# Optimization experiments

Hardware: AMD Instinct MI355X
Metric: run time of the kernel (lower is better)

Reference implementation:

```python
import jax, jax.numpy as jnp
import numpy as np

NUM_EXPERTS = 8
TOP_K = 2
HIDDEN = 768
FFN = 3072
B, S = 4, 4096


def setup_inputs() -> dict:
    key = jax.random.key(0)
    ks = jax.random.split(key, 7)
    scale_h = 1.0 / np.sqrt(HIDDEN)
    scale_f = 1.0 / np.sqrt(FFN)
    return {
        "hidden_states": jax.random.normal(ks[0], (B, S, HIDDEN), dtype=jnp.float32),
        "router_w": jax.random.normal(ks[1], (HIDDEN, NUM_EXPERTS), dtype=jnp.float32) * scale_h,
        "router_b": jnp.zeros((NUM_EXPERTS,), dtype=jnp.float32),
        "w1": jax.random.normal(ks[2], (NUM_EXPERTS, HIDDEN, FFN), dtype=jnp.float32) * scale_h,
        "b1": jnp.zeros((NUM_EXPERTS, FFN), dtype=jnp.float32),
        "w2": jax.random.normal(ks[3], (NUM_EXPERTS, FFN, HIDDEN), dtype=jnp.float32) * scale_f,
        "b2": jnp.zeros((NUM_EXPERTS, HIDDEN), dtype=jnp.float32),
    }


def _moe_forward(x_flat, router_w, router_b, w1, b1, w2, b2):
    T = x_flat.shape[0]
    # Router: logits [T, E]
    router_logits = x_flat @ router_w + router_b
    routing_weights = jax.nn.softmax(router_logits, axis=-1)
    # Top-k gating: softmax over the selected top-k logits
    top_vals, top_idx = jax.lax.top_k(router_logits, TOP_K)
    top_gates = jax.nn.softmax(top_vals, axis=-1)
    # Scatter gates into dense dispatch mask [T, E]
    rows = jnp.arange(T)[:, None]
    dispatch_mask = jnp.zeros_like(routing_weights).at[rows, top_idx].set(top_gates)
    # Expert computation: combined = sum_e gate[:, e] * FFN_e(x)
    # (tokens with zero gate contribute exactly 0, matching the torch scatter-combine)
    combined = jnp.zeros_like(x_flat)
    for e in range(NUM_EXPERTS):
        h = jax.nn.gelu(x_flat @ w1[e] + b1[e])  # [T, FFN]
        y = h @ w2[e] + b2[e]                    # [T, HIDDEN]
        combined = combined + dispatch_mask[:, e:e + 1] * y
    # Auxiliary load-balancing loss
    mean_routing_prob = jnp.mean(routing_weights, axis=0)
    tokens_per_expert = jnp.sum(dispatch_mask, axis=0) / T
    aux_loss = jnp.sum(mean_routing_prob * tokens_per_expert) * NUM_EXPERTS
    return combined, routing_weights, dispatch_mask, aux_loss, router_logits


def reference(hidden_states, router_w, router_b, w1, b1, w2, b2):
    batch, seq, hid = hidden_states.shape
    x_flat = hidden_states.reshape(-1, hid)
    combined, routing_weights, dispatch_mask, aux_loss, router_logits = _moe_forward(
        x_flat, router_w, router_b, w1, b1, w2, b2)
    E = NUM_EXPERTS
    return (
        combined.reshape(batch, seq, hid),            # expert_outputs
        routing_weights.reshape(batch, seq, E),       # routing_weights
        dispatch_mask.reshape(batch, seq, E),         # dispatch_mask
        aux_loss,                                     # aux_loss
        router_logits.reshape(batch, seq, E),         # router_logits
    )
```

## Files before the change

kernel.cpp:

```cpp
#include <hip/hip_runtime.h>
#include <math.h>

#define TOKENS 16384
#define HID 768
#define FFN_DIM 3072
#define NEXP 8
#define MAXT 136

#define RT_TPB 128
#define RT_BLOCKS (TOKENS / RT_TPB)

typedef __bf16 bf16x8 __attribute__((ext_vector_type(8)));
typedef float f32x4 __attribute__((ext_vector_type(4)));

#define GLOBAL_AS(p) ((const __attribute__((address_space(1))) void*)(p))
#define LDS_AS(p)    ((__attribute__((address_space(3))) void*)(p))

__device__ __forceinline__ float gelu_f(float x) {
    const float x3 = x * x * x;
    const float z = 0.7978845608028654f * (x + 0.044715f * x3);
    const float e = __expf(2.f * z);
    const float t = 1.f - 2.f / (e + 1.f);
    return 0.5f * x * (1.f + t);
}

__device__ __forceinline__ unsigned short f2bf(float v) {
    return __builtin_bit_cast(unsigned short, (__bf16)v);
}

__global__ void __launch_bounds__(512) router_kernel(
    const float* __restrict__ x, const float* __restrict__ rw,
    const float* __restrict__ rb,
    float* __restrict__ out_rw, float* __restrict__ out_dm,
    float* __restrict__ out_logits,
    int* __restrict__ counts, float* __restrict__ probsum,
    float* __restrict__ gatesum, int* __restrict__ lists,
    float* __restrict__ glists)
{
    __shared__ int s_cnt[NEXP], s_base[NEXP];
    __shared__ float s_prob[NEXP], s_gate[NEXP];
    __shared__ int s_e1[RT_TPB], s_s1[RT_TPB], s_e2[RT_TPB], s_s2[RT_TPB];
    __shared__ float s_g1v[RT_TPB], s_g2v[RT_TPB];

    const int tid = threadIdx.x;
    if (tid < NEXP) { s_cnt[tid] = 0; s_prob[tid] = 0.f; s_gate[tid] = 0.f; }
    __syncthreads();

    const int wave = tid >> 6, lane = tid & 63;

    for (int it = 0; it < RT_TPB / 8; ++it) {
        const int lt = wave * (RT_TPB / 8) + it;
        const int t = blockIdx.x * RT_TPB + lt;
        const float* xr = x + (size_t)t * HID;
        float acc[NEXP];
#pragma unroll
        for (int e = 0; e < NEXP; ++e) acc[e] = 0.f;
#pragma unroll
        for (int j = 0; j < 12; ++j) {
            const int i = lane + (j << 6);
            const float xv = xr[i];
            const float4 a = ((const float4*)(rw + (size_t)i * NEXP))[0];
            const float4 b = ((const float4*)(rw + (size_t)i * NEXP))[1];
            acc[0] += xv * a.x; acc[1] += xv * a.y; acc[2] += xv * a.z; acc[3] += xv * a.w;
            acc[4] += xv * b.x; acc[5] += xv * b.y; acc[6] += xv * b.z; acc[7] += xv * b.w;
        }
#pragma unroll
        for (int off = 32; off > 0; off >>= 1)
#pragma unroll
            for (int e = 0; e < NEXP; ++e) acc[e] += __shfl_down(acc[e], off, 64);

        if (lane == 0) {
            float lg[NEXP];
            float m = -1e30f;
#pragma unroll
            for (int e = 0; e < NEXP; ++e) { lg[e] = acc[e] + rb[e]; m = fmaxf(m, lg[e]); }
            float ex[NEXP]; float s = 0.f;
#pragma unroll
            for (int e = 0; e < NEXP; ++e) { ex[e] = expf(lg[e] - m); s += ex[e]; }
            const float inv = 1.f / s;
            float* lrow = out_logits + (size_t)t * NEXP;
            float* prow = out_rw + (size_t)t * NEXP;
#pragma unroll
            for (int e = 0; e < NEXP; ++e) {
                lrow[e] = lg[e];
                const float p = ex[e] * inv;
                prow[e] = p;
                atomicAdd(&s_prob[e], p);
            }
            int i1 = 0;
#pragma unroll
            for (int e = 1; e < NEXP; ++e) if (lg[e] > lg[i1]) i1 = e;
            int i2 = (i1 == 0) ? 1 : 0;
#pragma unroll
            for (int e = 0; e < NEXP; ++e) if (e != i1 && lg[e] > lg[i2]) i2 = e;
            const float e2 = expf(lg[i2] - lg[i1]);
            const float g1 = 1.f / (1.f + e2);
            const float g2 = e2 / (1.f + e2);
            out_dm[(size_t)t * NEXP + i1] = g1;
            out_dm[(size_t)t * NEXP + i2] = g2;
            atomicAdd(&s_gate[i1], g1);
            atomicAdd(&s_gate[i2], g2);
            s_e1[lt] = i1; s_s1[lt] = atomicAdd(&s_cnt[i1], 1); s_g1v[lt] = g1;
            s_e2[lt] = i2; s_s2[lt] = atomicAdd(&s_cnt[i2], 1); s_g2v[lt] = g2;
        }
    }
    __syncthreads();
    if (tid < NEXP) {
        s_base[tid] = atomicAdd(&counts[tid], s_cnt[tid]);
        atomicAdd(&probsum[tid], s_prob[tid]);
        atomicAdd(&gatesum[tid], s_gate[tid]);
    }
    __syncthreads();
    if (tid < RT_TPB) {
        const int t = blockIdx.x * RT_TPB + tid;
        int e = s_e1[tid]; int p = s_base[e] + s_s1[tid];
        lists[e * TOKENS + p] = t; glists[e * TOKENS + p] = s_g1v[tid];
        e = s_e2[tid]; p = s_base[e] + s_s2[tid];
        lists[e * TOKENS + p] = t; glists[e * TOKENS + p] = s_g2v[tid];
    }
}

__global__ void finalize_kernel(const int* __restrict__ counts,
                                const float* __restrict__ probsum,
                                const float* __restrict__ gatesum,
                                int* __restrict__ poffs,
                                float* __restrict__ out_aux)
{
    if (threadIdx.x == 0 && blockIdx.x == 0) {
        float s = 0.f; int po = 0;
        for (int e = 0; e < NEXP; ++e) {
            poffs[e] = po;
            po += ((counts[e] + 255) >> 8) << 8;
            s += (probsum[e] / (float)TOKENS) * (gatesum[e] / (float)TOKENS);
        }
        poffs[NEXP] = po;
        *out_aux = s * (float)NEXP;
    }
}

__global__ void __launch_bounds__(192) gatherx_kernel(
    const float* __restrict__ x, const int* __restrict__ counts,
    const int* __restrict__ poffs, const int* __restrict__ lists,
    unsigned short* __restrict__ Xg)
{
    const int r = blockIdx.x;
    if (r >= poffs[NEXP]) return;
    int e = 0;
#pragma unroll
    for (int q = 1; q < NEXP; ++q) e += (r >= poffs[q]);
    const int ri = r - poffs[e];
    const int tid = threadIdx.x;
    uint2 o = make_uint2(0u, 0u);
    if (ri < counts[e]) {
        const int tok = lists[e * TOKENS + ri];
        const float4 v = *(const float4*)&x[(size_t)tok * HID + tid * 4];
        o.x = (unsigned)f2bf(v.x) | ((unsigned)f2bf(v.y) << 16);
        o.y = (unsigned)f2bf(v.z) | ((unsigned)f2bf(v.w) << 16);
    }
    *(uint2*)&Xg[(size_t)r * HID + tid * 4] = o;
}

__global__ void __launch_bounds__(256) convT_kernel(const float* __restrict__ in,
                                                    unsigned short* __restrict__ out,
                                                    int R, int C)
{
    __shared__ float sT[32][65];
    const int e = blockIdx.z;
    const float* in_e = in + (size_t)e * R * C;
    unsigned short* out_e = out + (size_t)e * R * C;
    const int r0 = blockIdx.y * 64;
    const int c0 = blockIdx.x * 32;
    const int tid = threadIdx.x;
    const int rr = tid >> 3, c4 = (tid & 7) * 4;
#pragma unroll
    for (int half = 0; half < 2; ++half) {
        const int r = rr + half * 32;
        const float4 v = *(const float4*)&in_e[(size_t)(r0 + r) * C + c0 + c4];
        sT[c4 + 0][r] = v.x; sT[c4 + 1][r] = v.y;
        sT[c4 + 2][r] = v.z; sT[c4 + 3][r] = v.w;
    }
    __syncthreads();
    const int c = tid >> 3, u = tid & 7;
    uint4 pk;
    const float* sr = &sT[c][u * 8];
    pk.x = (unsigned)f2bf(sr[0]) | ((unsigned)f2bf(sr[1]) << 16);
    pk.y = (unsigned)f2bf(sr[2]) | ((unsigned)f2bf(sr[3]) << 16);
    pk.z = (unsigned)f2bf(sr[4]) | ((unsigned)f2bf(sr[5]) << 16);
    pk.w = (unsigned)f2bf(sr[6]) | ((unsigned)f2bf(sr[7]) << 16);
    *(uint4*)&out_e[(size_t)(c0 + c) * R + r0 + u * 8] = pk;
}


#define STAGE1(kt_) do { \
    _Pragma("unroll") \
    for (int _kh = 0; _kh < 2; ++_kh) { \
        const unsigned short* _pa = aStP + (kt_) * 64 + _kh * 32; \
        const unsigned short* _pb = bStP + (kt_) * 64 + _kh * 32; \
        __builtin_amdgcn_global_load_lds(GLOBAL_AS(_pa),           LDS_AS(aD + _kh * 4096),       16, 0, 0); \
        __builtin_amdgcn_global_load_lds(GLOBAL_AS(_pa + 16 * KS), LDS_AS(aD + _kh * 4096 + 512), 16, 0, 0); \
        __builtin_amdgcn_global_load_lds(GLOBAL_AS(_pb),           LDS_AS(bD + _kh * 4096),       16, 0, 0); \
        __builtin_amdgcn_global_load_lds(GLOBAL_AS(_pb + 16 * KS), LDS_AS(bD + _kh * 4096 + 512), 16, 0, 0); \
    } \
} while (0)

#define DECODE_TILE(NT_, MT_) \
    const int nwg = gridDim.x;                                                       \
    const int orig = blockIdx.x;                                                     \
    const int qq = nwg >> 3, rr2 = nwg & 7;                                          \
    const int xcd = orig & 7, pos = orig >> 3;                                       \
    const int wid = (xcd < rr2 ? xcd * (qq + 1) : rr2 * (qq + 1) + (xcd - rr2) * qq) + pos; \
    const int nSuper = (MT_) >> 3;                                                   \
    const int fullB = nSuper * 8 * (NT_);                                            \
    int mt, nti;                                                                     \
    if (wid < fullB) {                                                               \
        const int st_ = wid / (8 * (NT_));                                           \
        const int lo = wid - st_ * (8 * (NT_));                                      \
        mt = (st_ << 3) + (lo & 7);                                                  \
        nti = lo >> 3;                                                               \
    } else {                                                                         \
        const int rem = (MT_) - (nSuper << 3);                                       \
        const int lo = wid - fullB;                                                  \
        mt = (nSuper << 3) + lo % rem;                                               \
        nti = lo / rem;                                                              \
    }

__global__ void __launch_bounds__(256, 3) gemm1_kernel(
    const unsigned short* __restrict__ Xg, const unsigned short* __restrict__ W1T,
    const float* __restrict__ b1, const int* __restrict__ poffs,
    unsigned short* __restrict__ H, int grBase, int mtCount)
{
    __shared__ __bf16 sA[8192];
    __shared__ __bf16 sB[8192];
    const int KS = HID;
    const int NKT = HID / 64;

    DECODE_TILE(FFN_DIM / 128, mtCount)
    const int gr = grBase + mt * 128;
    if (gr >= poffs[NEXP]) return;
    int e = 0;
#pragma unroll
    for (int q = 1; q < NEXP; ++q) e += (gr >= poffs[q]);
    const int hbase = gr - grBase;
    const int n0 = nti * 128;

    const int tid = threadIdx.x;
    const int wv = tid >> 6, lane = tid & 63;
    const int wm = (wv >> 1) * 64, wn = (wv & 1) * 64;
    const int fr = lane & 15, q4 = lane >> 4;
    const int rowoff = lane >> 2;
    const int swzW = ((lane & 3) ^ ((lane >> 3) & 3)) << 3;
    const int swzR = (q4 ^ ((fr >> 1) & 3)) << 3;

    const unsigned short* aStP = Xg + (size_t)(gr + wv * 32 + rowoff) * KS + swzW;
    const unsigned short* bStP = W1T + (size_t)e * (HID * FFN_DIM)
                               + (size_t)(n0 + wv * 32 + rowoff) * KS + swzW;
    __bf16* aD = sA + wv * 1024;
    __bf16* bD = sB + wv * 1024;

    f32x4 acc[4][4];
#pragma unroll
    for (int a = 0; a < 4; ++a)
#pragma unroll
        for (int b = 0; b < 4; ++b) acc[a][b] = (f32x4)(0.f);

    for (int kt = 0; kt < NKT; ++kt) {
        STAGE1(kt);
        __syncthreads();
#pragma unroll
        for (int kh = 0; kh < 2; ++kh) {
            bf16x8 af[4], bb[4];
#pragma unroll
            for (int t = 0; t < 4; ++t) {
                af[t] = *(const bf16x8*)&sA[kh * 4096 + (wm + t * 16 + fr) * 32 + swzR];
                bb[t] = *(const bf16x8*)&sB[kh * 4096 + (wn + t * 16 + fr) * 32 + swzR];
            }
#pragma unroll
            for (int tm = 0; tm < 4; ++tm)
#pragma unroll
                for (int tn = 0; tn < 4; ++tn)
                    acc[tm][tn] = __builtin_amdgcn_mfma_f32_16x16x32_bf16(
                        af[tm], bb[tn], acc[tm][tn], 0, 0, 0);
        }
        __syncthreads();
    }

    const float* b1e = b1 + (size_t)e * FFN_DIM;
    float bias[4];
#pragma unroll
    for (int tn = 0; tn < 4; ++tn) bias[tn] = b1e[n0 + wn + tn * 16 + fr];
#pragma unroll
    for (int tm = 0; tm < 4; ++tm) {
#pragma unroll
        for (int tn = 0; tn < 4; ++tn) {
            const int n = n0 + wn + tn * 16 + fr;
#pragma unroll
            for (int r = 0; r < 4; ++r) {
                const int mloc = wm + tm * 16 + q4 * 4 + r;
                const float h = gelu_f(acc[tm][tn][r] + bias[tn]);
                H[(size_t)(hbase + mloc) * FFN_DIM + n] = f2bf(h);
            }
        }
    }
}

__global__ void __launch_bounds__(256, 3) gemm2_kernel(
    const unsigned short* __restrict__ H, const unsigned short* __restrict__ W2T,
    const float* __restrict__ b2, const int* __restrict__ counts,
    const int* __restrict__ poffs, const int* __restrict__ lists,
    const float* __restrict__ glists, float* __restrict__ out,
    int grBase, int mtCount)
{
    __shared__ __bf16 sA[8192];
    __shared__ __bf16 sB[8192];
    __shared__ int sTok[128];
    __shared__ float sGate[128];
    const int KS = FFN_DIM;
    const int NKT = FFN_DIM / 64;

    DECODE_TILE(HID / 128, mtCount)
    const int gr = grBase + mt * 128;
    if (gr >= poffs[NEXP]) return;
    int e = 0;
#pragma unroll
    for (int q = 1; q < NEXP; ++q) e += (gr >= poffs[q]);
    const int cnt = counts[e];
    const int m0 = gr - poffs[e];
    const int hbase = gr - grBase;
    const int n0 = nti * 128;

    const int tid = threadIdx.x;
    const int wv = tid >> 6, lane = tid & 63;
    const int wm = (wv >> 1) * 64, wn = (wv & 1) * 64;
    const int fr = lane & 15, q4 = lane >> 4;
    const int rowoff = lane >> 2;
    const int swzW = ((lane & 3) ^ ((lane >> 3) & 3)) << 3;
    const int swzR = (q4 ^ ((fr >> 1) & 3)) << 3;

    if (tid < 128) {
        int ri = m0 + tid; if (ri > cnt - 1) ri = cnt - 1;
        sTok[tid] = lists[e * TOKENS + ri];
        sGate[tid] = glists[e * TOKENS + ri];
    }

    const unsigned short* aStP = H + (size_t)(hbase + wv * 32 + rowoff) * KS + swzW;
    const unsigned short* bStP = W2T + (size_t)e * (HID * FFN_DIM)
                               + (size_t)(n0 + wv * 32 + rowoff) * KS + swzW;
    __bf16* aD = sA + wv * 1024;
    __bf16* bD = sB + wv * 1024;

    f32x4 acc[4][4];
#pragma unroll
    for (int a = 0; a < 4; ++a)
#pragma unroll
        for (int b = 0; b < 4; ++b) acc[a][b] = (f32x4)(0.f);

    for (int kt = 0; kt < NKT; ++kt) {
        STAGE1(kt);
        __syncthreads();
#pragma unroll
        for (int kh = 0; kh < 2; ++kh) {
            bf16x8 af[4], bb[4];
#pragma unroll
            for (int t = 0; t < 4; ++t) {
                af[t] = *(const bf16x8*)&sA[kh * 4096 + (wm + t * 16 + fr) * 32 + swzR];
                bb[t] = *(const bf16x8*)&sB[kh * 4096 + (wn + t * 16 + fr) * 32 + swzR];
            }
#pragma unroll
            for (int tm = 0; tm < 4; ++tm)
#pragma unroll
                for (int tn = 0; tn < 4; ++tn)
                    acc[tm][tn] = __builtin_amdgcn_mfma_f32_16x16x32_bf16(
                        af[tm], bb[tn], acc[tm][tn], 0, 0, 0);
        }
        __syncthreads();
    }

    const float* b2e = b2 + (size_t)e * HID;
    float bias[4];
#pragma unroll
    for (int tn = 0; tn < 4; ++tn) bias[tn] = b2e[n0 + wn + tn * 16 + fr];
#pragma unroll
    for (int tm = 0; tm < 4; ++tm) {
#pragma unroll
        for (int tn = 0; tn < 4; ++tn) {
            const int n = n0 + wn + tn * 16 + fr;
#pragma unroll
            for (int r = 0; r < 4; ++r) {
                const int mloc = wm + tm * 16 + q4 * 4 + r;
                if (m0 + mloc < cnt) {
                    const float y = acc[tm][tn][r] + bias[tn];
                    atomicAdd(&out[(size_t)sTok[mloc] * HID + n], sGate[mloc] * y);
                }
            }
        }
    }
}

#define BM 16
#define KC 64
#define XS 772
#define HS 68
__global__ void __launch_bounds__(256) ffn_kernel(
    const float* __restrict__ x, const float* __restrict__ w1,
    const float* __restrict__ b1, const float* __restrict__ w2,
    const float* __restrict__ b2, const int* __restrict__ counts,
    const int* __restrict__ lists, const float* __restrict__ glists,
    float* __restrict__ out)
{
    const int e = blockIdx.y;
    const int count = counts[e];
    const int row0 = blockIdx.x * BM;
    if (row0 >= count) return;

    __shared__ float sX[BM * XS];
    __shared__ float sH[BM * HS];
    __shared__ int sTokF[BM];
    __shared__ float sGateF[BM];
    const int tid = threadIdx.x;

    if (tid < BM) {
        const int ri = row0 + tid;
        int tok = 0; float g = 0.f;
        if (ri < count) { tok = lists[e * TOKENS + ri]; g = glists[e * TOKENS + ri]; }
        sTokF[tid] = tok; sGateF[tid] = g;
    }
    __syncthreads();
    {
        const int r = tid >> 4, q = tid & 15;
        const float4* src = (const float4*)(x + (size_t)sTokF[r] * HID);
#pragma unroll
        for (int j = 0; j < 12; ++j) {
            const float4 v = src[q + (j << 4)];
            *(float4*)&sX[r * XS + ((q + (j << 4)) << 2)] = v;
        }
    }
    __syncthreads();

    const float* w1e = w1 + (size_t)e * HID * FFN_DIM;
    const float* w2e = w2 + (size_t)e * FFN_DIM * HID;
    const float* b1e = b1 + (size_t)e * FFN_DIM;
    const float* b2e = b2 + (size_t)e * HID;
    const int r1 = tid & 15;
    const int c0 = (tid >> 4) << 2;
    const int c2 = (tid >> 4) * 48;

    float Y[48];
#pragma unroll
    for (int j = 0; j < 48; ++j) Y[j] = 0.f;

    for (int ch = 0; ch < FFN_DIM / KC; ++ch) {
        float h0 = 0.f, h1 = 0.f, h2 = 0.f, h3 = 0.f;
        const float* w1c = w1e + ch * KC + c0;
        for (int i = 0; i < HID; i += 4) {
            const float4 xv = *(const float4*)&sX[r1 * XS + i];
            const float* wp = w1c + (size_t)i * FFN_DIM;
            const float4 wa = *(const float4*)(wp);
            const float4 wb = *(const float4*)(wp + FFN_DIM);
            const float4 wc = *(const float4*)(wp + 2 * FFN_DIM);
            const float4 wd = *(const float4*)(wp + 3 * FFN_DIM);
            h0 += xv.x * wa.x + xv.y * wb.x + xv.z * wc.x + xv.w * wd.x;
            h1 += xv.x * wa.y + xv.y * wb.y + xv.z * wc.y + xv.w * wd.y;
            h2 += xv.x * wa.z + xv.y * wb.z + xv.z * wc.z + xv.w * wd.z;
            h3 += xv.x * wa.w + xv.y * wb.w + xv.z * wc.w + xv.w * wd.w;
        }
        const int cb = ch * KC + c0;
        h0 = gelu_f(h0 + b1e[cb + 0]);
        h1 = gelu_f(h1 + b1e[cb + 1]);
        h2 = gelu_f(h2 + b1e[cb + 2]);
        h3 = gelu_f(h3 + b1e[cb + 3]);
        __syncthreads();
        *(float4*)&sH[r1 * HS + c0] = make_float4(h0, h1, h2, h3);
        __syncthreads();
        const float* w2c = w2e + (size_t)ch * KC * HID + c2;
        for (int k = 0; k < KC; ++k) {
            const float hv = sH[r1 * HS + k];
            const float4* wr = (const float4*)(w2c + (size_t)k * HID);
#pragma unroll
            for (int j4 = 0; j4 < 12; ++j4) {
                const float4 wv = wr[j4];
                Y[j4 * 4 + 0] += hv * wv.x;
                Y[j4 * 4 + 1] += hv * wv.y;
                Y[j4 * 4 + 2] += hv * wv.z;
                Y[j4 * 4 + 3] += hv * wv.w;
            }
        }
    }
    const int ri = row0 + r1;
    if (ri < count) {
        const float g = sGateF[r1];
        float* orow = out + (size_t)sTokF[r1] * HID + c2;
#pragma unroll
        for (int j = 0; j < 48; ++j)
            atomicAdd(&orow[j], g * (Y[j] + b2e[c2 + j]));
    }
}

extern "C" void kernel_launch(void* const* d_in, const int* in_sizes, int n_in,
                              void* d_out, int out_size, void* d_ws, size_t ws_size,
                              hipStream_t stream)
{
    const float* x  = (const float*)d_in[0];
    const float* rw = (const float*)d_in[1];
    const float* rb = (const float*)d_in[2];
    const float* w1 = (const float*)d_in[3];
    const float* b1 = (const float*)d_in[4];
    const float* w2 = (const float*)d_in[5];
    const float* b2 = (const float*)d_in[6];

    float* out = (float*)d_out;
    float* out_comb   = out;
    float* out_rw     = out + (size_t)TOKENS * HID;
    float* out_dm     = out_rw + (size_t)TOKENS * NEXP;
    float* out_aux    = out_dm + (size_t)TOKENS * NEXP;
    float* out_logits = out_aux + 1;

    char* ws = (char*)d_ws;
    int*   counts  = (int*)ws;
    int*   poffs   = (int*)(ws + 64);
    float* probsum = (float*)(ws + 128);
    float* gatesum = (float*)(ws + 160);
    int*   lists   = (int*)(ws + 256);
    float* glists  = (float*)(ws + 256 + (size_t)NEXP * TOKENS * 4);
    size_t off = 256 + (size_t)NEXP * TOKENS * 8;
    off = (off + 255) & ~(size_t)255;
    unsigned short* Xg  = (unsigned short*)(ws + off); off += (size_t)MAXT * 256 * HID * 2;
    unsigned short* W1T = (unsigned short*)(ws + off); off += (size_t)NEXP * HID * FFN_DIM * 2;
    unsigned short* W2T = (unsigned short*)(ws + off); off += (size_t)NEXP * HID * FFN_DIM * 2;
    unsigned short* Hbuf = (unsigned short*)(ws + off);

    size_t avail = (ws_size > off) ? (ws_size - off) : 0;
    const int tilesFit = (int)(avail / ((size_t)256 * FFN_DIM * 2));
    int G = 0, tilesPG = 0;
    if (tilesFit >= 1) {
        G = (MAXT + tilesFit - 1) / tilesFit;
        tilesPG = (MAXT + G - 1) / G;
    }

    hipMemsetAsync(out_comb, 0, (size_t)TOKENS * HID * sizeof(float), stream);
    hipMemsetAsync(out_dm, 0, (size_t)TOKENS * NEXP * sizeof(float), stream);
    hipMemsetAsync(d_ws, 0, 256, stream);

    router_kernel<<<dim3(RT_BLOCKS), 512, 0, stream>>>(
        x, rw, rb, out_rw, out_dm, out_logits,
        counts, probsum, gatesum, lists, glists);
    finalize_kernel<<<1, 64, 0, stream>>>(counts, probsum, gatesum, poffs, out_aux);

    if (G > 0) {
        gatherx_kernel<<<dim3(MAXT * 256), 192, 0, stream>>>(
            x, counts, poffs, lists, Xg);
        convT_kernel<<<dim3(FFN_DIM / 32, HID / 64, NEXP), 256, 0, stream>>>(w1, W1T, HID, FFN_DIM);
        convT_kernel<<<dim3(HID / 32, FFN_DIM / 64, NEXP), 256, 0, stream>>>(w2, W2T, FFN_DIM, HID);
        for (int g = 0; g < G; ++g) {
            const int grBase = g * tilesPG * 256;
            const int mtCount = tilesPG * 2;
            gemm1_kernel<<<dim3(mtCount * (FFN_DIM / 128)), 256, 0, stream>>>(
                Xg, W1T, b1, poffs, Hbuf, grBase, mtCount);
            gemm2_kernel<<<dim3(mtCount * (HID / 128)), 256, 0, stream>>>(
                Hbuf, W2T, b2, counts, poffs, lists, glists, out_comb, grBase, mtCount);
        }
    } else {
        ffn_kernel<<<dim3(TOKENS / BM, NEXP), 256, 0, stream>>>(
            x, w1, b1, w2, b2, counts, lists, glists, out_comb);
    }
}
```

Before: 838.8 us.

## Double-buffer LDS tiles in expert GEMMs to overlap loads with MFMA

Both expert GEMM kernels now use a two-stage LDS ping-pong held in dynamic shared memory. The next K tile is issued via global_load_lds before the MFMA work on the current tile, which removes one barrier per iteration and hides global-load latency. In exchange LDS use doubles to 64KB+ per block and the launch-bounds occupancy hint drops from 3 to 2 blocks per CU. The kernels also need a one-time hipFuncSetAttribute call to allow the larger dynamic LDS.

```diff
diff --git a/kernel.cpp b/kernel.cpp
--- a/kernel.cpp
+++ b/kernel.cpp
@@ -191,15 +191,33 @@
 }
 
 
-#define STAGE1(kt_) do { \
+#define STAGE1(bufE_, kt_) do { \
     _Pragma("unroll") \
     for (int _kh = 0; _kh < 2; ++_kh) { \
         const unsigned short* _pa = aStP + (kt_) * 64 + _kh * 32; \
         const unsigned short* _pb = bStP + (kt_) * 64 + _kh * 32; \
-        __builtin_amdgcn_global_load_lds(GLOBAL_AS(_pa),           LDS_AS(aD + _kh * 4096),       16, 0, 0); \
-        __builtin_amdgcn_global_load_lds(GLOBAL_AS(_pa + 16 * KS), LDS_AS(aD + _kh * 4096 + 512), 16, 0, 0); \
-        __builtin_amdgcn_global_load_lds(GLOBAL_AS(_pb),           LDS_AS(bD + _kh * 4096),       16, 0, 0); \
-        __builtin_amdgcn_global_load_lds(GLOBAL_AS(_pb + 16 * KS), LDS_AS(bD + _kh * 4096 + 512), 16, 0, 0); \
+        __builtin_amdgcn_global_load_lds(GLOBAL_AS(_pa),           LDS_AS(aD + (bufE_) + _kh * 4096),       16, 0, 0); \
+        __builtin_amdgcn_global_load_lds(GLOBAL_AS(_pa + 16 * KS), LDS_AS(aD + (bufE_) + _kh * 4096 + 512), 16, 0, 0); \
+        __builtin_amdgcn_global_load_lds(GLOBAL_AS(_pb),           LDS_AS(bD + (bufE_) + _kh * 4096),       16, 0, 0); \
+        __builtin_amdgcn_global_load_lds(GLOBAL_AS(_pb + 16 * KS), LDS_AS(bD + (bufE_) + _kh * 4096 + 512), 16, 0, 0); \
+    } \
+} while (0)
+
+#define COMPUTE_TILE(curE_) do { \
+    _Pragma("unroll") \
+    for (int kh = 0; kh < 2; ++kh) { \
+        bf16x8 af[4], bb[4]; \
+        _Pragma("unroll") \
+        for (int t = 0; t < 4; ++t) { \
+            af[t] = *(const bf16x8*)&lds[(curE_) + kh * 4096 + (wm + t * 16 + fr) * 32 + swzR]; \
+            bb[t] = *(const bf16x8*)&lds[16384 + (curE_) + kh * 4096 + (wn + t * 16 + fr) * 32 + swzR]; \
+        } \
+        _Pragma("unroll") \
+        for (int tm = 0; tm < 4; ++tm) \
+            _Pragma("unroll") \
+            for (int tn = 0; tn < 4; ++tn) \
+                acc[tm][tn] = __builtin_amdgcn_mfma_f32_16x16x32_bf16( \
+                    af[tm], bb[tn], acc[tm][tn], 0, 0, 0); \
     } \
 } while (0)
 
@@ -224,13 +242,12 @@
         nti = lo / rem;                                                              \
     }
 
-__global__ void __launch_bounds__(256, 3) gemm1_kernel(
+__global__ void __launch_bounds__(256, 2) gemm1_kernel(
     const unsigned short* __restrict__ Xg, const unsigned short* __restrict__ W1T,
     const float* __restrict__ b1, const int* __restrict__ poffs,
     unsigned short* __restrict__ H, int grBase, int mtCount)
 {
-    __shared__ __bf16 sA[8192];
-    __shared__ __bf16 sB[8192];
+    extern __shared__ __bf16 lds[];
     const int KS = HID;
     const int NKT = HID / 64;
 
@@ -254,8 +271,8 @@
     const unsigned short* aStP = Xg + (size_t)(gr + wv * 32 + rowoff) * KS + swzW;
     const unsigned short* bStP = W1T + (size_t)e * (HID * FFN_DIM)
                                + (size_t)(n0 + wv * 32 + rowoff) * KS + swzW;
-    __bf16* aD = sA + wv * 1024;
-    __bf16* bD = sB + wv * 1024;
+    __bf16* aD = lds + wv * 1024;
+    __bf16* bD = lds + 16384 + wv * 1024;
 
     f32x4 acc[4][4];
 #pragma unroll
@@ -263,24 +280,13 @@
 #pragma unroll
         for (int b = 0; b < 4; ++b) acc[a][b] = (f32x4)(0.f);
 
+    STAGE1(0, 0);
+    __syncthreads();
+#pragma unroll 2
     for (int kt = 0; kt < NKT; ++kt) {
-        STAGE1(kt);
-        __syncthreads();
-#pragma unroll
-        for (int kh = 0; kh < 2; ++kh) {
-            bf16x8 af[4], bb[4];
-#pragma unroll
-            for (int t = 0; t < 4; ++t) {
-                af[t] = *(const bf16x8*)&sA[kh * 4096 + (wm + t * 16 + fr) * 32 + swzR];
-                bb[t] = *(const bf16x8*)&sB[kh * 4096 + (wn + t * 16 + fr) * 32 + swzR];
-            }
-#pragma unroll
-            for (int tm = 0; tm < 4; ++tm)
-#pragma unroll
-                for (int tn = 0; tn < 4; ++tn)
-                    acc[tm][tn] = __builtin_amdgcn_mfma_f32_16x16x32_bf16(
-                        af[tm], bb[tn], acc[tm][tn], 0, 0, 0);
-        }
+        const int curE = (kt & 1) * 8192;
+        if (kt + 1 < NKT) STAGE1(8192 - curE, kt + 1);
+        COMPUTE_TILE(curE);
         __syncthreads();
     }
 
@@ -303,17 +309,14 @@
     }
 }
 
-__global__ void __launch_bounds__(256, 3) gemm2_kernel(
+__global__ void __launch_bounds__(256, 2) gemm2_kernel(
     const unsigned short* __restrict__ H, const unsigned short* __restrict__ W2T,
     const float* __restrict__ b2, const int* __restrict__ counts,
     const int* __restrict__ poffs, const int* __restrict__ lists,
     const float* __restrict__ glists, float* __restrict__ out,
     int grBase, int mtCount)
 {
-    __shared__ __bf16 sA[8192];
-    __shared__ __bf16 sB[8192];
-    __shared__ int sTok[128];
-    __shared__ float sGate[128];
+    extern __shared__ __bf16 lds[];
     const int KS = FFN_DIM;
     const int NKT = FFN_DIM / 64;
 
@@ -327,6 +330,9 @@
     const int m0 = gr - poffs[e];
     const int hbase = gr - grBase;
     const int n0 = nti * 128;
+
+    int* sTok = (int*)&lds[32768];
+    float* sGate = (float*)&lds[33024];
 
     const int tid = threadIdx.x;
     const int wv = tid >> 6, lane = tid & 63;
@@ -345,8 +351,8 @@
     const unsigned short* aStP = H + (size_t)(hbase + wv * 32 + rowoff) * KS + swzW;
     const unsigned short* bStP = W2T + (size_t)e * (HID * FFN_DIM)
                                + (size_t)(n0 + wv * 32 + rowoff) * KS + swzW;
-    __bf16* aD = sA + wv * 1024;
-    __bf16* bD = sB + wv * 1024;
+    __bf16* aD = lds + wv * 1024;
+    __bf16* bD = lds + 16384 + wv * 1024;
 
     f32x4 acc[4][4];
 #pragma unroll
@@ -354,24 +360,13 @@
 #pragma unroll
         for (int b = 0; b < 4; ++b) acc[a][b] = (f32x4)(0.f);
 
+    STAGE1(0, 0);
+    __syncthreads();
+#pragma unroll 2
     for (int kt = 0; kt < NKT; ++kt) {
-        STAGE1(kt);
-        __syncthreads();
-#pragma unroll
-        for (int kh = 0; kh < 2; ++kh) {
-            bf16x8 af[4], bb[4];
-#pragma unroll
-            for (int t = 0; t < 4; ++t) {
-                af[t] = *(const bf16x8*)&sA[kh * 4096 + (wm + t * 16 + fr) * 32 + swzR];
-                bb[t] = *(const bf16x8*)&sB[kh * 4096 + (wn + t * 16 + fr) * 32 + swzR];
-            }
-#pragma unroll
-            for (int tm = 0; tm < 4; ++tm)
-#pragma unroll
-                for (int tn = 0; tn < 4; ++tn)
-                    acc[tm][tn] = __builtin_amdgcn_mfma_f32_16x16x32_bf16(
-                        af[tm], bb[tn], acc[tm][tn], 0, 0, 0);
-        }
+        const int curE = (kt & 1) * 8192;
+        if (kt + 1 < NKT) STAGE1(8192 - curE, kt + 1);
+        COMPUTE_TILE(curE);
         __syncthreads();
     }
 
@@ -546,6 +541,14 @@
     finalize_kernel<<<1, 64, 0, stream>>>(counts, probsum, gatesum, poffs, out_aux);
 
     if (G > 0) {
+        static int attr_done = 0;
+        if (!attr_done) {
+            hipFuncSetAttribute((const void*)gemm1_kernel,
+                                hipFuncAttributeMaxDynamicSharedMemorySize, 65536);
+            hipFuncSetAttribute((const void*)gemm2_kernel,
+                                hipFuncAttributeMaxDynamicSharedMemorySize, 66560);
+            attr_done = 1;
+        }
         gatherx_kernel<<<dim3(MAXT * 256), 192, 0, stream>>>(
             x, counts, poffs, lists, Xg);
         convT_kernel<<<dim3(FFN_DIM / 32, HID / 64, NEXP), 256, 0, stream>>>(w1, W1T, HID, FFN_DIM);
@@ -553,9 +556,9 @@
         for (int g = 0; g < G; ++g) {
             const int grBase = g * tilesPG * 256;
             const int mtCount = tilesPG * 2;
-            gemm1_kernel<<<dim3(mtCount * (FFN_DIM / 128)), 256, 0, stream>>>(
+            gemm1_kernel<<<dim3(mtCount * (FFN_DIM / 128)), 256, 65536, stream>>>(
                 Xg, W1T, b1, poffs, Hbuf, grBase, mtCount);
-            gemm2_kernel<<<dim3(mtCount * (HID / 128)), 256, 0, stream>>>(
+            gemm2_kernel<<<dim3(mtCount * (HID / 128)), 256, 66560, stream>>>(
                 Hbuf, W2T, b2, counts, poffs, lists, glists, out_comb, grBase, mtCount);
         }
     } else {
```

New measurement: 881.4 us. 5.1% more time.
